# Performance work log

Measured on AMD Instinct MI355X. Metric: run time of the kernel, lower is better.

Reference implementation:

```python
import jax, jax.numpy as jnp
import numpy as np

NEG_INF = -1e30
N, L, D2, ATTN, T = 32, 2048, 1024, 512, 8  # D2 = 2*dim


def setup_inputs() -> dict:
    key = jax.random.key(0)
    ks = jax.random.split(key, 16)
    s = 0.02
    return {
        "encoder_outputs": jax.random.normal(ks[0], (N, L, D2), jnp.float32),
        "h0": jax.random.normal(ks[1], (N, D2), jnp.float32),
        "c0": jax.random.normal(ks[2], (N, D2), jnp.float32),
        "mask": jax.random.randint(ks[3], (N, L), 0, 2, jnp.int32),
        "W_ih": jax.random.normal(ks[4], (4 * D2, D2), jnp.float32) * s,
        "W_hh": jax.random.normal(ks[5], (4 * D2, D2), jnp.float32) * s,
        "b_ih": jax.random.normal(ks[6], (4 * D2,), jnp.float32) * s,
        "b_hh": jax.random.normal(ks[7], (4 * D2,), jnp.float32) * s,
        "W1": jax.random.normal(ks[8], (ATTN, D2), jnp.float32) * s,
        "b1": jax.random.normal(ks[9], (ATTN,), jnp.float32) * s,
        "W2": jax.random.normal(ks[10], (ATTN, D2), jnp.float32) * s,
        "b2": jax.random.normal(ks[11], (ATTN,), jnp.float32) * s,
        "w3": jax.random.normal(ks[12], (ATTN,), jnp.float32) * s,
        "b3": jax.random.normal(ks[13], (), jnp.float32) * s,
    }


def _lstm_cell(x, h, c, W_ih, W_hh, b_ih, b_hh):
    gates = x @ W_ih.T + b_ih + h @ W_hh.T + b_hh  # [N, 4*D2]
    i, f, g, o = jnp.split(gates, 4, axis=-1)      # torch gate order i,f,g,o
    i, f, o = jax.nn.sigmoid(i), jax.nn.sigmoid(f), jax.nn.sigmoid(o)
    g = jnp.tanh(g)
    c_new = f * c + i * g
    h_new = o * jnp.tanh(c_new)
    return h_new, c_new


def reference(encoder_outputs, h0, c0, mask, W_ih, W_hh, b_ih, b_hh, W1, b1, W2, b2, w3, b3):
    maskf = mask.astype(encoder_outputs.dtype)
    # loop-invariant: linear2(encoder_outputs), hoisted out of the decode loop
    enc_proj = jnp.einsum('nld,ad->nla', encoder_outputs, W2) + b2  # [N,L,ATTN]
    mask_add = (1.0 - maskf) * NEG_INF                              # [N,L]
    x_init = jnp.zeros_like(h0)

    def step(carry, _):
        x, h, c = carry
        h, c = _lstm_cell(x, h, c, W_ih, W_hh, b_ih, b_hh)
        q = h @ W1.T + b1                                           # [N,ATTN]
        attn = jnp.tanh(q[:, None, :] + enc_proj) @ w3 + b3         # [N,L]
        attn = attn + mask_add
        p = jax.nn.softmax(attn, axis=-1)
        x_next = jnp.einsum('nl,nld->nd', p, encoder_outputs)       # attended input
        return (x_next, h, c), attn

    _, attns = jax.lax.scan(step, (x_init, h0, c0), None, length=T)
    return jnp.transpose(attns, (1, 0, 2))  # [N, T, L]
```

## Files before the change

kernel.cpp:

```cpp
#include <hip/hip_runtime.h>

#define NB 32
#define LL 2048
#define DD 1024
#define AA 512
#define TT 8
#define LOG2E 1.4426950408889634f

typedef short short8 __attribute__((ext_vector_type(8)));
typedef float f32x4 __attribute__((ext_vector_type(4)));

#if __has_builtin(__builtin_amdgcn_exp2f)
#define EXP2(x) __builtin_amdgcn_exp2f(x)
#else
#define EXP2(x) exp2f(x)
#endif
#if __has_builtin(__builtin_amdgcn_rcpf)
#define RCP(x) __builtin_amdgcn_rcpf(x)
#else
#define RCP(x) (1.0f/(x))
#endif

__device__ __forceinline__ unsigned short f2b(float f){
  union { float f; unsigned u; } v; v.f = f;
  unsigned r = v.u + 0x7fffu + ((v.u >> 16) & 1u);
  return (unsigned short)(r >> 16);
}
__device__ __forceinline__ float b2f(unsigned short b){
  union { unsigned u; float f; } v; v.u = ((unsigned)b) << 16;
  return v.f;
}
__device__ __forceinline__ float sigm(float x){
  return RCP(1.f + EXP2(-x * LOG2E));
}
__device__ __forceinline__ float tanh_f(float x){
  return 2.f * RCP(1.f + EXP2(-2.f * LOG2E * x)) - 1.f;
}
__device__ __forceinline__ void gll16(const unsigned short* g, void* l){
  __builtin_amdgcn_global_load_lds(
      (const __attribute__((address_space(1))) unsigned int*)(g),
      (__attribute__((address_space(3))) unsigned int*)(l),
      16, 0, 0);
}

__device__ __forceinline__ unsigned char sw_enc_e4m3(float f){
  union{float f;unsigned u;} v; v.f = f;
  unsigned s = (v.u>>31)<<7;
  float a = fabsf(f);
  if (a < 0.015625f){
    int q = (int)(a*512.f + 0.5f);
    if (q > 7) return s | (1<<3);
    return s | q;
  }
  int e = ((v.u>>23)&255) - 127;
  unsigned m = ((v.u & 0x7FFFFF) + 0x80000) >> 20;
  if (m == 8){ m = 0; e++; }
  int eb = e + 7;
  if (eb > 15){ eb = 15; m = 6; }
  if (eb <= 0){
    int q = (int)(a*512.f + 0.5f); if (q>7) q=7;
    return s | q;
  }
  return s | (eb<<3) | m;
}
__device__ __forceinline__ unsigned char f2e8(float f){
#if __has_builtin(__builtin_amdgcn_cvt_pk_fp8_f32)
  return (unsigned char)(__builtin_amdgcn_cvt_pk_fp8_f32(f, f, 0, false) & 0xFF);
#else
  return sw_enc_e4m3(f);
#endif
}
__device__ __forceinline__ float sw_dec_e4m3(unsigned char c){
  unsigned s = c>>7, e = (c>>3)&15, m = c&7;
  if (e){ union{unsigned u;float f;} x; x.u = (s<<31)|((e+120)<<23)|(m<<20); return x.f; }
  float r = (float)m * 0.001953125f;
  return s ? -r : r;
}
#if __has_builtin(__builtin_amdgcn_cvt_f32_fp8)
#define DEC8(word, sel) __builtin_amdgcn_cvt_f32_fp8((int)(word), (sel))
#else
#define DEC8(word, sel) sw_dec_e4m3((unsigned char)(((word) >> ((sel)*8)) & 0xFF))
#endif

__global__ __launch_bounds__(256) void k_cvt_enc(const float* __restrict__ in,
                                                 unsigned short* __restrict__ ob,
                                                 unsigned char* __restrict__ o8,
                                                 long n8){
  long stride = (long)gridDim.x * 256;
  for (long i = (long)blockIdx.x*256 + threadIdx.x; i < n8; i += stride){
    const float4* ip = (const float4*)(in + i*8);
    float4 a = ip[0], b = ip[1];
    uint4 o;
    o.x = (unsigned)f2b(a.x) | ((unsigned)f2b(a.y) << 16);
    o.y = (unsigned)f2b(a.z) | ((unsigned)f2b(a.w) << 16);
    o.z = (unsigned)f2b(b.x) | ((unsigned)f2b(b.y) << 16);
    o.w = (unsigned)f2b(b.z) | ((unsigned)f2b(b.w) << 16);
    *(uint4*)(ob + i*8) = o;
    uint2 p;
    p.x = (unsigned)f2e8(a.x) | ((unsigned)f2e8(a.y)<<8) |
          ((unsigned)f2e8(a.z)<<16) | ((unsigned)f2e8(a.w)<<24);
    p.y = (unsigned)f2e8(b.x) | ((unsigned)f2e8(b.y)<<8) |
          ((unsigned)f2e8(b.z)<<16) | ((unsigned)f2e8(b.w)<<24);
    *(uint2*)(o8 + i*8) = p;
  }
}

__global__ __launch_bounds__(256) void k_cvt4(
    const float* __restrict__ s0, const float* __restrict__ s1,
    const float* __restrict__ s2, const float* __restrict__ s3,
    unsigned short* __restrict__ d0, unsigned short* __restrict__ d1,
    unsigned short* __restrict__ d2, unsigned short* __restrict__ d3,
    long c0, long c1, long c2, long c3)
{
  long i = (long)blockIdx.x*256 + threadIdx.x;
  const float* s; unsigned short* d; long idx = i;
  if (idx < c0){ s = s0; d = d0; }
  else { idx -= c0;
    if (idx < c1){ s = s1; d = d1; }
    else { idx -= c1;
      if (idx < c2){ s = s2; d = d2; }
      else { idx -= c2; if (idx >= c3) return; s = s3; d = d3; } } }
  const float4* ip = (const float4*)(s + idx*8);
  float4 a = ip[0], b = ip[1];
  uint4 o;
  o.x = (unsigned)f2b(a.x) | ((unsigned)f2b(a.y) << 16);
  o.y = (unsigned)f2b(a.z) | ((unsigned)f2b(a.w) << 16);
  o.z = (unsigned)f2b(b.x) | ((unsigned)f2b(b.y) << 16);
  o.w = (unsigned)f2b(b.z) | ((unsigned)f2b(b.w) << 16);
  *(uint4*)(d + idx*8) = o;
}

__global__ __launch_bounds__(256) void k_gemm_encproj(
    const unsigned short* __restrict__ A,
    const unsigned short* __restrict__ Bt,
    const float* __restrict__ b2,
    unsigned char* __restrict__ C8)
{
  __shared__ unsigned short As[128*32];
  __shared__ unsigned short Bs[128*32];
  const int tid = threadIdx.x;
  const int wid = tid >> 6, lane = tid & 63;
  const int wm = wid >> 1, wn = wid & 1;
  const int hi = lane >> 4, r = lane & 15;
  const long brow = (long)blockIdx.x * 128;
  const int bcol = blockIdx.y * 128;
  const int srow = wid*32 + (lane >> 2);
  const int scol = (lane & 3) * 8;
  const unsigned short* aS0 = A + (brow + srow)*1024 + scol;
  const unsigned short* aS1 = A + (brow + srow + 16)*1024 + scol;
  const unsigned short* bS0 = Bt + (long)(bcol + srow)*1024 + scol;
  const unsigned short* bS1 = Bt + (long)(bcol + srow + 16)*1024 + scol;
  char* aD = (char*)As + wid*2048;
  char* bD = (char*)Bs + wid*2048;

  f32x4 acc[4][4];
  #pragma unroll
  for (int i=0;i<4;i++)
    #pragma unroll
    for (int j=0;j<4;j++) acc[i][j] = (f32x4){0.f,0.f,0.f,0.f};

  for (int k0 = 0; k0 < 1024; k0 += 32){
    __syncthreads();
    gll16(aS0 + k0, aD);
    gll16(aS1 + k0, aD + 1024);
    gll16(bS0 + k0, bD);
    gll16(bS1 + k0, bD + 1024);
    __syncthreads();
    short8 af[4], bfr[4];
    #pragma unroll
    for (int fm=0; fm<4; fm++)
      af[fm] = *(const short8*)((const char*)As + (wm*64 + fm*16 + r)*64 + hi*16);
    #pragma unroll
    for (int fn=0; fn<4; fn++)
      bfr[fn] = *(const short8*)((const char*)Bs + (wn*64 + fn*16 + r)*64 + hi*16);
    #pragma unroll
    for (int fm=0; fm<4; fm++)
      #pragma unroll
      for (int fn=0; fn<4; fn++)
        acc[fm][fn] = __builtin_amdgcn_mfma_f32_16x16x32_bf16(af[fm], bfr[fn], acc[fm][fn], 0, 0, 0);
  }
  #pragma unroll
  for (int fm=0; fm<4; fm++){
    #pragma unroll
    for (int fn=0; fn<4; fn++){
      int col = bcol + wn*64 + fn*16 + r;
      float bias = b2[col];
      #pragma unroll
      for (int q=0; q<4; q++){
        long row = brow + wm*64 + fm*16 + hi*4 + q;
        C8[row*512 + col] = f2e8(acc[fm][fn][q] + bias);
      }
    }
  }
}

__global__ __launch_bounds__(256) void k_glstm(
    const float* __restrict__ x, const float* __restrict__ h_in,
    const float* __restrict__ c_in,
    const unsigned short* __restrict__ Wih, const unsigned short* __restrict__ Whh,
    const float* __restrict__ b_ih, const float* __restrict__ b_hh,
    float* __restrict__ h_out, float* __restrict__ c_out, int first)
{
  const int wid = threadIdx.x >> 6, lane = threadIdx.x & 63;
  const int d = (blockIdx.x >> 1)*4 + wid;
  const int n0 = (blockIdx.x & 1) << 4;
  float wi[4][16], wh[4][16], bias[4];
  #pragma unroll
  for (int g=0; g<4; g++){
    const int rg = g*1024 + d;
    const long wo = (long)rg*1024 + lane*16;
    short8 a0 = *(const short8*)(Wih + wo);
    short8 a1 = *(const short8*)(Wih + wo + 8);
    short8 h0v = *(const short8*)(Whh + wo);
    short8 h1v = *(const short8*)(Whh + wo + 8);
    #pragma unroll
    for (int i=0;i<8;i++){
      wi[g][i]   = b2f((unsigned short)a0[i]);  wi[g][i+8] = b2f((unsigned short)a1[i]);
      wh[g][i]   = b2f((unsigned short)h0v[i]); wh[g][i+8] = b2f((unsigned short)h1v[i]);
    }
    bias[g] = b_ih[rg] + b_hh[rg];
  }
  for (int n=n0; n<n0+16; n++){
    const float4* hp = (const float4*)(h_in + n*1024 + lane*16);
    float ha[16];
    *(float4*)(ha+0)=hp[0]; *(float4*)(ha+4)=hp[1]; *(float4*)(ha+8)=hp[2]; *(float4*)(ha+12)=hp[3];
    float s0=0.f, s1=0.f, s2=0.f, s3=0.f;
    if (first){
      #pragma unroll
      for (int i=0;i<16;i++){
        s0 += ha[i]*wh[0][i]; s1 += ha[i]*wh[1][i];
        s2 += ha[i]*wh[2][i]; s3 += ha[i]*wh[3][i];
      }
    } else {
      const float4* xp = (const float4*)(x + n*1024 + lane*16);
      float xa[16];
      *(float4*)(xa+0)=xp[0]; *(float4*)(xa+4)=xp[1]; *(float4*)(xa+8)=xp[2]; *(float4*)(xa+12)=xp[3];
      #pragma unroll
      for (int i=0;i<16;i++){
        s0 += xa[i]*wi[0][i] + ha[i]*wh[0][i];
        s1 += xa[i]*wi[1][i] + ha[i]*wh[1][i];
        s2 += xa[i]*wi[2][i] + ha[i]*wh[2][i];
        s3 += xa[i]*wi[3][i] + ha[i]*wh[3][i];
      }
    }
    #pragma unroll
    for (int o=32;o>0;o>>=1){
      s0 += __shfl_xor(s0, o); s1 += __shfl_xor(s1, o);
      s2 += __shfl_xor(s2, o); s3 += __shfl_xor(s3, o);
    }
    if (lane == 0){
      const int idx = n*1024 + d;
      float gi = sigm(s0 + bias[0]);
      float gf = sigm(s1 + bias[1]);
      float gg = tanh_f(s2 + bias[2]);
      float go = sigm(s3 + bias[3]);
      float cn = gf*c_in[idx] + gi*gg;
      c_out[idx] = cn;
      h_out[idx] = go * tanh_f(cn);
    }
  }
}

__global__ __launch_bounds__(256) void k_q(
    const float* __restrict__ h, const unsigned short* __restrict__ W1,
    const float* __restrict__ b1, float* __restrict__ q)
{
  const int wid = threadIdx.x >> 6, lane = threadIdx.x & 63;
  const int jgrp = blockIdx.x >> 1;
  const int n0 = (blockIdx.x & 1) << 4;
  const int j0 = (jgrp*4 + wid)*2;
  float wf[2][16], bias[2];
  #pragma unroll
  for (int jj=0;jj<2;jj++){
    const long wo = (long)(j0+jj)*1024 + lane*16;
    short8 w0 = *(const short8*)(W1 + wo);
    short8 w1 = *(const short8*)(W1 + wo + 8);
    #pragma unroll
    for (int i=0;i<8;i++){ wf[jj][i] = b2f((unsigned short)w0[i]); wf[jj][i+8] = b2f((unsigned short)w1[i]); }
    bias[jj] = b1[j0+jj];
  }
  for (int n=n0; n<n0+16; n++){
    const float4* hp = (const float4*)(h + n*1024 + lane*16);
    float ha[16];
    *(float4*)(ha+0)=hp[0]; *(float4*)(ha+4)=hp[1]; *(float4*)(ha+8)=hp[2]; *(float4*)(ha+12)=hp[3];
    float s0=0.f, s1=0.f;
    #pragma unroll
    for (int i=0;i<16;i++){ s0 += ha[i]*wf[0][i]; s1 += ha[i]*wf[1][i]; }
    #pragma unroll
    for (int o=32;o>0;o>>=1){ s0 += __shfl_xor(s0, o); s1 += __shfl_xor(s1, o); }
    if (lane == 0){ q[n*AA + j0] = s0 + bias[0]; q[n*AA + j0 + 1] = s1 + bias[1]; }
  }
}

__global__ __launch_bounds__(256) void k_attnx(
    const unsigned char* __restrict__ ep8, const float* __restrict__ qv,
    const float* __restrict__ w3, const float* __restrict__ b3p,
    const int* __restrict__ mask, const unsigned char* __restrict__ enc8,
    float* __restrict__ out, float* __restrict__ part,
    float* __restrict__ psum, int t)
{
  const int n = blockIdx.y, ch = blockIdx.x;
  const int tid = threadIdx.x;
  const int wid = tid >> 6, lane = tid & 63;
  __shared__ float p_s[64];

  float qf[8], w3f[8];
  const float4* qp = (const float4*)(qv + n*AA + lane*8);
  *(float4*)(qf+0) = qp[0]; *(float4*)(qf+4) = qp[1];
  const float4* wp = (const float4*)(w3 + lane*8);
  *(float4*)(w3f+0) = wp[0]; *(float4*)(w3f+4) = wp[1];
  const float b3v = b3p[0];

  #pragma unroll 1
  for (int li = 0; li < 16; li++){
    const int l = ch*64 + wid*16 + li;
    uint2 e = *(const uint2*)(ep8 + ((long)n*LL + l)*AA + lane*8);
    float ef[8];
    ef[0]=DEC8(e.x,0); ef[1]=DEC8(e.x,1); ef[2]=DEC8(e.x,2); ef[3]=DEC8(e.x,3);
    ef[4]=DEC8(e.y,0); ef[5]=DEC8(e.y,1); ef[6]=DEC8(e.y,2); ef[7]=DEC8(e.y,3);
    float s = 0.f;
    #pragma unroll
    for (int i=0;i<8;i++) s += tanh_f(ef[i] + qf[i]) * w3f[i];
    #pragma unroll
    for (int o=32;o>0;o>>=1) s += __shfl_xor(s, o);
    if (lane == 0){
      float a = s + b3v;
      int mk = mask[n*LL + l];
      float aout = a;
      if (!mk) aout += -1e30f;
      out[((long)n*TT + t)*LL + l] = aout;
      p_s[wid*16 + li] = mk ? EXP2(a*LOG2E) : 0.f;
    }
  }
  __syncthreads();

  const unsigned char* base = enc8 + ((long)n*LL + ch*64)*1024 + tid*4;
  float a0=0.f, a1=0.f, a2=0.f, a3=0.f;
  #pragma unroll 4
  for (int li=0; li<64; li++){
    float pv = p_s[li];
    unsigned u = *(const unsigned*)(base + (long)li*1024);
    a0 = fmaf(pv, DEC8(u,0), a0);
    a1 = fmaf(pv, DEC8(u,1), a1);
    a2 = fmaf(pv, DEC8(u,2), a2);
    a3 = fmaf(pv, DEC8(u,3), a3);
  }
  float4 o = {a0,a1,a2,a3};
  *(float4*)(part + ((long)(n*32+ch))*1024 + tid*4) = o;
  if (tid == 0){
    float S = 0.f;
    #pragma unroll
    for (int i=0;i<64;i++) S += p_s[i];
    psum[n*32 + ch] = S;
  }
}

__global__ __launch_bounds__(256) void k_xreduce(const float* __restrict__ part,
                                                 const float* __restrict__ psum,
                                                 float* __restrict__ x){
  int idx = blockIdx.x*256 + threadIdx.x;
  int n = idx >> 10, d = idx & 1023;
  float S = 0.f;
  #pragma unroll
  for (int ch=0; ch<32; ch++) S += psum[n*32 + ch];
  float s = 0.f;
  #pragma unroll
  for (int ch=0; ch<32; ch++) s += part[((long)(n*32+ch))*1024 + d];
  x[idx] = s * RCP(S);
}

extern "C" void kernel_launch(void* const* d_in, const int* in_sizes, int n_in,
                              void* d_out, int out_size, void* d_ws, size_t ws_size,
                              hipStream_t stream){
  const float* enc_f = (const float*)d_in[0];
  const float* h0    = (const float*)d_in[1];
  const float* c0    = (const float*)d_in[2];
  const int*   mask  = (const int*)d_in[3];
  const float* Wih_f = (const float*)d_in[4];
  const float* Whh_f = (const float*)d_in[5];
  const float* b_ih  = (const float*)d_in[6];
  const float* b_hh  = (const float*)d_in[7];
  const float* W1_f  = (const float*)d_in[8];
  const float* b1    = (const float*)d_in[9];
  const float* W2_f  = (const float*)d_in[10];
  const float* b2    = (const float*)d_in[11];
  const float* w3    = (const float*)d_in[12];
  const float* b3    = (const float*)d_in[13];
  float* out = (float*)d_out;

  char* ws = (char*)d_ws;
  size_t off = 0;
  auto alloc = [&](size_t bytes){ void* p = ws + off; off += (bytes + 255) & ~255ull; return p; };
  unsigned short* enc_b = (unsigned short*)alloc((size_t)NB*LL*DD*2);
  unsigned char*  enc_8 = (unsigned char*)alloc((size_t)NB*LL*DD);
  unsigned char*  ep_8  = (unsigned char*)alloc((size_t)NB*LL*AA);
  unsigned short* Wih_b = (unsigned short*)alloc((size_t)4*DD*DD*2);
  unsigned short* Whh_b = (unsigned short*)alloc((size_t)4*DD*DD*2);
  unsigned short* W1_b  = (unsigned short*)alloc((size_t)AA*DD*2);
  unsigned short* W2_b  = (unsigned short*)alloc((size_t)AA*DD*2);
  float* hA    = (float*)alloc((size_t)NB*DD*4);
  float* hB    = (float*)alloc((size_t)NB*DD*4);
  float* cbuf  = (float*)alloc((size_t)NB*DD*4);
  float* xbuf  = (float*)alloc((size_t)NB*DD*4);
  float* qbuf  = (float*)alloc((size_t)NB*AA*4);
  float* part  = (float*)alloc((size_t)NB*32*DD*4);
  float* psum  = (float*)alloc((size_t)NB*32*4);

  k_cvt_enc<<<4096,256,0,stream>>>(enc_f, enc_b, enc_8, (long)NB*LL*DD/8);
  k_cvt4<<<4608,256,0,stream>>>(Wih_f, Whh_f, W1_f, W2_f,
                                Wih_b, Whh_b, W1_b, W2_b,
                                (long)4*DD*DD/8, (long)4*DD*DD/8,
                                (long)AA*DD/8, (long)AA*DD/8);
  k_gemm_encproj<<<dim3(512,4),256,0,stream>>>(enc_b, W2_b, b2, ep_8);

  float* hcur = hA; float* hnxt = hB;
  for (int t=0; t<TT; t++){
    k_glstm<<<512,256,0,stream>>>(xbuf,
                                  t==0 ? h0 : hcur,
                                  t==0 ? c0 : cbuf,
                                  Wih_b, Whh_b, b_ih, b_hh,
                                  hnxt, cbuf, t==0 ? 1 : 0);
    k_q<<<128,256,0,stream>>>(hnxt, W1_b, b1, qbuf);
    k_attnx<<<dim3(32,NB),256,0,stream>>>(ep_8, qbuf, w3, b3, mask, enc_8,
                                          out, part, psum, t);
    k_xreduce<<<128,256,0,stream>>>(part, psum, xbuf);
    float* tmp = hcur; hcur = hnxt; hnxt = tmp;
  }
}
```

Before: 732.2 us.

## Run encoder projection GEMM in FP8 and drop the bf16 encoder copy

The encoder projection GEMM now reads the existing e4m3 encoder copy and an e4m3 version of W2 (pre-scaled by 32 to stay out of the subnormal range), using fp8 MFMA with the scale undone in the epilogue. This removes the bf16 encoder conversion and its write, which is a large buffer (32×2048×1024×2 bytes), and halves the GEMM's input bytes. The cost is lower precision in the attention projection, which may shift the attention logits.

Result: faster. 697.3 us (-4.8%).

```diff
diff --git a/kernel.cpp b/kernel.cpp
--- a/kernel.cpp
+++ b/kernel.cpp
@@ -36,7 +36,7 @@
 __device__ __forceinline__ float tanh_f(float x){
   return 2.f * RCP(1.f + EXP2(-2.f * LOG2E * x)) - 1.f;
 }
-__device__ __forceinline__ void gll16(const unsigned short* g, void* l){
+__device__ __forceinline__ void gll16(const void* g, void* l){
   __builtin_amdgcn_global_load_lds(
       (const __attribute__((address_space(1))) unsigned int*)(g),
       (__attribute__((address_space(3))) unsigned int*)(l),
@@ -83,19 +83,12 @@
 #endif
 
 __global__ __launch_bounds__(256) void k_cvt_enc(const float* __restrict__ in,
-                                                 unsigned short* __restrict__ ob,
                                                  unsigned char* __restrict__ o8,
                                                  long n8){
   long stride = (long)gridDim.x * 256;
   for (long i = (long)blockIdx.x*256 + threadIdx.x; i < n8; i += stride){
     const float4* ip = (const float4*)(in + i*8);
     float4 a = ip[0], b = ip[1];
-    uint4 o;
-    o.x = (unsigned)f2b(a.x) | ((unsigned)f2b(a.y) << 16);
-    o.y = (unsigned)f2b(a.z) | ((unsigned)f2b(a.w) << 16);
-    o.z = (unsigned)f2b(b.x) | ((unsigned)f2b(b.y) << 16);
-    o.w = (unsigned)f2b(b.z) | ((unsigned)f2b(b.w) << 16);
-    *(uint4*)(ob + i*8) = o;
     uint2 p;
     p.x = (unsigned)f2e8(a.x) | ((unsigned)f2e8(a.y)<<8) |
           ((unsigned)f2e8(a.z)<<16) | ((unsigned)f2e8(a.w)<<24);
@@ -109,17 +102,29 @@
     const float* __restrict__ s0, const float* __restrict__ s1,
     const float* __restrict__ s2, const float* __restrict__ s3,
     unsigned short* __restrict__ d0, unsigned short* __restrict__ d1,
-    unsigned short* __restrict__ d2, unsigned short* __restrict__ d3,
+    unsigned short* __restrict__ d2, unsigned char* __restrict__ d3,
     long c0, long c1, long c2, long c3)
 {
   long i = (long)blockIdx.x*256 + threadIdx.x;
-  const float* s; unsigned short* d; long idx = i;
+  long idx = i;
+  const float* s; unsigned short* d;
   if (idx < c0){ s = s0; d = d0; }
   else { idx -= c0;
     if (idx < c1){ s = s1; d = d1; }
     else { idx -= c1;
       if (idx < c2){ s = s2; d = d2; }
-      else { idx -= c2; if (idx >= c3) return; s = s3; d = d3; } } }
+      else {
+        idx -= c2; if (idx >= c3) return;
+        const float4* ip = (const float4*)(s3 + idx*8);
+        float4 a = ip[0], b = ip[1];
+        uint2 p;
+        p.x = (unsigned)f2e8(a.x*32.f) | ((unsigned)f2e8(a.y*32.f)<<8) |
+              ((unsigned)f2e8(a.z*32.f)<<16) | ((unsigned)f2e8(a.w*32.f)<<24);
+        p.y = (unsigned)f2e8(b.x*32.f) | ((unsigned)f2e8(b.y*32.f)<<8) |
+              ((unsigned)f2e8(b.z*32.f)<<16) | ((unsigned)f2e8(b.w*32.f)<<24);
+        *(uint2*)(d3 + idx*8) = p;
+        return;
+      } } }
   const float4* ip = (const float4*)(s + idx*8);
   float4 a = ip[0], b = ip[1];
   uint4 o;
@@ -130,14 +135,14 @@
   *(uint4*)(d + idx*8) = o;
 }
 
-__global__ __launch_bounds__(256) void k_gemm_encproj(
-    const unsigned short* __restrict__ A,
-    const unsigned short* __restrict__ Bt,
+__global__ __launch_bounds__(256) void k_gemm8(
+    const unsigned char* __restrict__ A,
+    const unsigned char* __restrict__ Bt,
     const float* __restrict__ b2,
     unsigned char* __restrict__ C8)
 {
-  __shared__ unsigned short As[128*32];
-  __shared__ unsigned short Bs[128*32];
+  __shared__ unsigned char As[128*64];
+  __shared__ unsigned char Bs[128*64];
   const int tid = threadIdx.x;
   const int wid = tid >> 6, lane = tid & 63;
   const int wm = wid >> 1, wn = wid & 1;
@@ -145,11 +150,11 @@
   const long brow = (long)blockIdx.x * 128;
   const int bcol = blockIdx.y * 128;
   const int srow = wid*32 + (lane >> 2);
-  const int scol = (lane & 3) * 8;
-  const unsigned short* aS0 = A + (brow + srow)*1024 + scol;
-  const unsigned short* aS1 = A + (brow + srow + 16)*1024 + scol;
-  const unsigned short* bS0 = Bt + (long)(bcol + srow)*1024 + scol;
-  const unsigned short* bS1 = Bt + (long)(bcol + srow + 16)*1024 + scol;
+  const int scol = (lane & 3) * 16;
+  const unsigned char* aS0 = A + (brow + srow)*1024 + scol;
+  const unsigned char* aS1 = A + (brow + srow + 16)*1024 + scol;
+  const unsigned char* bS0 = Bt + (long)(bcol + srow)*1024 + scol;
+  const unsigned char* bS1 = Bt + (long)(bcol + srow + 16)*1024 + scol;
   char* aD = (char*)As + wid*2048;
   char* bD = (char*)Bs + wid*2048;
 
@@ -159,26 +164,33 @@
     #pragma unroll
     for (int j=0;j<4;j++) acc[i][j] = (f32x4){0.f,0.f,0.f,0.f};
 
-  for (int k0 = 0; k0 < 1024; k0 += 32){
+  for (int k0 = 0; k0 < 1024; k0 += 64){
     __syncthreads();
     gll16(aS0 + k0, aD);
     gll16(aS1 + k0, aD + 1024);
     gll16(bS0 + k0, bD);
     gll16(bS1 + k0, bD + 1024);
     __syncthreads();
-    short8 af[4], bfr[4];
-    #pragma unroll
-    for (int fm=0; fm<4; fm++)
-      af[fm] = *(const short8*)((const char*)As + (wm*64 + fm*16 + r)*64 + hi*16);
-    #pragma unroll
-    for (int fn=0; fn<4; fn++)
-      bfr[fn] = *(const short8*)((const char*)Bs + (wn*64 + fn*16 + r)*64 + hi*16);
+    long af[4][2], bfr[4][2];
+    #pragma unroll
+    for (int fm=0; fm<4; fm++){
+      af[fm][0] = *(const long*)((const char*)As + (wm*64 + fm*16 + r)*64 + hi*8);
+      af[fm][1] = *(const long*)((const char*)As + (wm*64 + fm*16 + r)*64 + 32 + hi*8);
+    }
+    #pragma unroll
+    for (int fn=0; fn<4; fn++){
+      bfr[fn][0] = *(const long*)((const char*)Bs + (wn*64 + fn*16 + r)*64 + hi*8);
+      bfr[fn][1] = *(const long*)((const char*)Bs + (wn*64 + fn*16 + r)*64 + 32 + hi*8);
+    }
     #pragma unroll
     for (int fm=0; fm<4; fm++)
       #pragma unroll
-      for (int fn=0; fn<4; fn++)
-        acc[fm][fn] = __builtin_amdgcn_mfma_f32_16x16x32_bf16(af[fm], bfr[fn], acc[fm][fn], 0, 0, 0);
-  }
+      for (int fn=0; fn<4; fn++){
+        acc[fm][fn] = __builtin_amdgcn_mfma_f32_16x16x32_fp8_fp8(af[fm][0], bfr[fn][0], acc[fm][fn], 0, 0, 0);
+        acc[fm][fn] = __builtin_amdgcn_mfma_f32_16x16x32_fp8_fp8(af[fm][1], bfr[fn][1], acc[fm][fn], 0, 0, 0);
+      }
+  }
+  const float inv32 = 1.f/32.f;
   #pragma unroll
   for (int fm=0; fm<4; fm++){
     #pragma unroll
@@ -188,7 +200,7 @@
       #pragma unroll
       for (int q=0; q<4; q++){
         long row = brow + wm*64 + fm*16 + hi*4 + q;
-        C8[row*512 + col] = f2e8(acc[fm][fn][q] + bias);
+        C8[row*512 + col] = f2e8(acc[fm][fn][q]*inv32 + bias);
       }
     }
   }
@@ -391,13 +403,12 @@
   char* ws = (char*)d_ws;
   size_t off = 0;
   auto alloc = [&](size_t bytes){ void* p = ws + off; off += (bytes + 255) & ~255ull; return p; };
-  unsigned short* enc_b = (unsigned short*)alloc((size_t)NB*LL*DD*2);
   unsigned char*  enc_8 = (unsigned char*)alloc((size_t)NB*LL*DD);
   unsigned char*  ep_8  = (unsigned char*)alloc((size_t)NB*LL*AA);
   unsigned short* Wih_b = (unsigned short*)alloc((size_t)4*DD*DD*2);
   unsigned short* Whh_b = (unsigned short*)alloc((size_t)4*DD*DD*2);
   unsigned short* W1_b  = (unsigned short*)alloc((size_t)AA*DD*2);
-  unsigned short* W2_b  = (unsigned short*)alloc((size_t)AA*DD*2);
+  unsigned char*  W2_8  = (unsigned char*)alloc((size_t)AA*DD);
   float* hA    = (float*)alloc((size_t)NB*DD*4);
   float* hB    = (float*)alloc((size_t)NB*DD*4);
   float* cbuf  = (float*)alloc((size_t)NB*DD*4);
@@ -406,12 +417,12 @@
   float* part  = (float*)alloc((size_t)NB*32*DD*4);
   float* psum  = (float*)alloc((size_t)NB*32*4);
 
-  k_cvt_enc<<<4096,256,0,stream>>>(enc_f, enc_b, enc_8, (long)NB*LL*DD/8);
+  k_cvt_enc<<<4096,256,0,stream>>>(enc_f, enc_8, (long)NB*LL*DD/8);
   k_cvt4<<<4608,256,0,stream>>>(Wih_f, Whh_f, W1_f, W2_f,
-                                Wih_b, Whh_b, W1_b, W2_b,
+                                Wih_b, Whh_b, W1_b, W2_8,
                                 (long)4*DD*DD/8, (long)4*DD*DD/8,
                                 (long)AA*DD/8, (long)AA*DD/8);
-  k_gemm_encproj<<<dim3(512,4),256,0,stream>>>(enc_b, W2_b, b2, ep_8);
+  k_gemm8<<<dim3(512,4),256,0,stream>>>(enc_8, W2_8, b2, ep_8);
 
   float* hcur = hA; float* hnxt = hB;
   for (int t=0; t<TT; t++){
```
